# Performance work log

Hardware: AMD Instinct MI355X
Metric: run time of the kernel (lower is better)

The kernel has to match this reference:

```python
import jax, jax.numpy as jnp
import numpy as np

NUM_HEAD = 16
D = 1024
HEAD_DIM = D // NUM_HEAD
EPS = 1e-5


def setup_inputs() -> dict:
    key = jax.random.key(0)
    ks = jax.random.split(key, 7)
    B, S = 2, 2048
    s = 1.0 / np.sqrt(D)
    return {
        "x": jax.random.normal(ks[0], (B, S, D), dtype=jnp.float32),
        "wq": jax.random.uniform(ks[1], (D, D), jnp.float32, -s, s),
        "bq": jax.random.uniform(ks[2], (D,), jnp.float32, -s, s),
        "wk": jax.random.uniform(ks[3], (D, D), jnp.float32, -s, s),
        "bk": jax.random.uniform(ks[4], (D,), jnp.float32, -s, s),
        "wv": jax.random.uniform(ks[5], (D, D), jnp.float32, -s, s),
        "bv": jax.random.uniform(ks[6], (D,), jnp.float32, -s, s),
        "gamma": jnp.ones((D,), jnp.float32),
        "beta": jnp.zeros((D,), jnp.float32),
    }


def reference(x, wq, bq, wk, bk, wv, bv, gamma, beta):
    B, S, Dm = x.shape
    # Linear: x @ W^T + b (torch convention), then split heads -> [B, H, S, hd]
    def proj(w, b):
        y = jnp.einsum("bsd,ed->bse", x, w) + b
        return y.reshape(B, S, NUM_HEAD, HEAD_DIM).transpose(0, 2, 1, 3)

    q = proj(wq, bq)
    k = proj(wk, bk)
    v = proj(wv, bv)

    scores = jnp.einsum("bhqd,bhkd->bhqk", q, k) / np.sqrt(HEAD_DIM).astype(x.dtype)
    attn = jax.nn.softmax(scores, axis=-1)
    out = jnp.einsum("bhqk,bhkd->bhqd", attn, v)
    out = out.transpose(0, 2, 1, 3).reshape(B, S, Dm)

    out = out + x
    mu = jnp.mean(out, axis=-1, keepdims=True)
    var = jnp.var(out, axis=-1, keepdims=True)
    out = (out - mu) * jax.lax.rsqrt(var + EPS) * gamma + beta
    return out
```

## Files before the change

kernel.cpp:

```cpp
#include <hip/hip_runtime.h>

typedef unsigned short u16;
typedef unsigned int   u32;
typedef __bf16 bf16x8 __attribute__((ext_vector_type(8)));
typedef float  f32x4  __attribute__((ext_vector_type(4)));

#define D_MODEL 1024
#define SEQ     2048
#define NHEAD   16
#define HD      64
#define SOFTMAX_SCL 0.18033688011112042f

__device__ __forceinline__ u16 f2bf(float f) {
    u32 u;
    __builtin_memcpy(&u, &f, 4);
    u32 r = (u + 0x7fffu + ((u >> 16) & 1u)) >> 16;
    return (u16)r;
}
__device__ __forceinline__ float bf2f(u16 v) {
    u32 u = ((u32)v) << 16;
    float f;
    __builtin_memcpy(&f, &u, 4);
    return f;
}

__device__ __forceinline__ void async_copy16(const u16* g, u16* l) {
    __builtin_amdgcn_global_load_lds(
        (__attribute__((address_space(1))) void*)g,
        (__attribute__((address_space(3))) void*)l, 16, 0, 0);
}

__device__ __forceinline__ uint2 pack4(float a, float b, float c, float d) {
    uint2 r;
    r.x = (u32)f2bf(a) | ((u32)f2bf(b) << 16);
    r.y = (u32)f2bf(c) | ((u32)f2bf(d) << 16);
    return r;
}

#define NX4 ((2 * SEQ * D_MODEL) / 4)
#define NW4 ((D_MODEL * D_MODEL) / 4)
__global__ __launch_bounds__(256) void conv_all(
    const float* __restrict__ x,  const float* __restrict__ wq,
    const float* __restrict__ wk, const float* __restrict__ wv,
    u16* __restrict__ xb, u16* __restrict__ wqb,
    u16* __restrict__ wkb, u16* __restrict__ wvb)
{
    int i = blockIdx.x * 256 + threadIdx.x;
    const float* src; u16* dst; int off;
    if (i < NX4)            { src = x;  dst = xb;  off = i; }
    else if (i < NX4 + NW4) { src = wq; dst = wqb; off = i - NX4; }
    else if (i < NX4 + 2 * NW4) { src = wk; dst = wkb; off = i - NX4 - NW4; }
    else                    { src = wv; dst = wvb; off = i - NX4 - 2 * NW4; }
    float4 a = ((const float4*)src)[off];
    ushort4 o;
    o.x = f2bf(a.x); o.y = f2bf(a.y); o.z = f2bf(a.z); o.w = f2bf(a.w);
    ((ushort4*)dst)[off] = o;
}

__global__ __launch_bounds__(256) void qkv_gemm(
    const u16* __restrict__ xb,
    const u16* __restrict__ wqb, const float* __restrict__ bq,
    const u16* __restrict__ wkb, const float* __restrict__ bk,
    const u16* __restrict__ wvb, const float* __restrict__ bv,
    u16* __restrict__ qb, u16* __restrict__ kb, u16* __restrict__ vt)
{
    const int bid  = blockIdx.x;
    const int pair = bid % 24;
    const int by   = bid / 24;
    const int z    = pair >> 3;
    const int bx   = pair & 7;

    const u16* Ap; const u16* Bp;
    int m0, n0;
    if (z < 2) {
        Ap = (z == 1) ? wkb : wqb;  Bp = xb;
        m0 = bx * 128;
        n0 = by * 128;
    } else {
        Ap = xb;  Bp = wvb;
        m0 = by * 128;
        n0 = bx * 128;
    }

    __shared__ u16 As[128 * 64];
    __shared__ u16 Bs[128 * 64];

    const int tid  = threadIdx.x;
    const int wave = tid >> 6;
    const int lane = tid & 63;
    const int quad = lane >> 4;
    const int l16  = lane & 15;
    const int wm   = wave >> 1;
    const int wn   = wave & 1;
    const int swz  = l16 & 7;

    int rr[4], co[4];
#pragma unroll
    for (int t = 0; t < 4; ++t) {
        int ch = (wave * 4 + t) * 64 + lane;
        rr[t] = ch >> 3;
        co[t] = ((ch & 7) ^ (rr[t] & 7)) * 8;
    }

    f32x4 acc[4][4] = {};

    for (int kt = 0; kt < D_MODEL; kt += 64) {
        __syncthreads();
#pragma unroll
        for (int t = 0; t < 4; ++t) {
            int chbase = (wave * 4 + t) * 64;
            async_copy16(Ap + (size_t)(m0 + rr[t]) * D_MODEL + kt + co[t], As + chbase * 8);
            async_copy16(Bp + (size_t)(n0 + rr[t]) * D_MODEL + kt + co[t], Bs + chbase * 8);
        }
        __syncthreads();

#pragma unroll
        for (int kc = 0; kc < 2; ++kc) {
            bf16x8 af[4], bf_[4];
#pragma unroll
            for (int i = 0; i < 4; ++i)
                af[i] = *(const bf16x8*)&As[(wm * 64 + i * 16 + l16) * 64 + (((kc * 4 + quad) ^ swz) << 3)];
#pragma unroll
            for (int j = 0; j < 4; ++j)
                bf_[j] = *(const bf16x8*)&Bs[(wn * 64 + j * 16 + l16) * 64 + (((kc * 4 + quad) ^ swz) << 3)];
            __builtin_amdgcn_s_setprio(1);
#pragma unroll
            for (int i = 0; i < 4; ++i)
#pragma unroll
                for (int j = 0; j < 4; ++j)
                    acc[i][j] = __builtin_amdgcn_mfma_f32_16x16x32_bf16(af[i], bf_[j], acc[i][j], 0, 0, 0);
            __builtin_amdgcn_s_setprio(0);
        }
    }

    if (z < 2) {
        const int chunk_lo = (quad & 1) * 4;
        u16* out = (z == 1) ? kb : qb;
        const float* bi = (z == 1) ? bk : bq;
        const float scl = (z == 1) ? 1.0f : SOFTMAX_SCL;
        const int fblk = m0 + wm * 64;
#pragma unroll
        for (int i = 0; i < 4; ++i) {
            const int fb = fblk + i * 16 + quad * 4;
            float4 b4 = *(const float4*)&bi[fb];
            const int chunk = i * 2 + (quad >> 1);
#pragma unroll
            for (int j = 0; j < 4; ++j) {
                int token = n0 + wn * 64 + j * 16 + l16;
                uint2 pk = pack4((acc[i][j][0] + b4.x) * scl,
                                 (acc[i][j][1] + b4.y) * scl,
                                 (acc[i][j][2] + b4.z) * scl,
                                 (acc[i][j][3] + b4.w) * scl);
                size_t addr = (size_t)token * D_MODEL + fblk
                            + ((chunk ^ (token & 7)) << 3) + chunk_lo;
                *(uint2*)&out[addr] = pk;
            }
        }
    } else {
#pragma unroll
        for (int j = 0; j < 4; ++j) {
            int feat = n0 + wn * 64 + j * 16 + l16;
            float bias = bv[feat];
            int hh = feat >> 6, d = feat & 63;
            const size_t rowbase = ((size_t)hh * HD + d) * SEQ;
#pragma unroll
            for (int i = 0; i < 4; ++i) {
                int tok = m0 + wm * 64 + i * 16 + quad * 4;
                int b = tok >> 11, s = tok & 2047;
                const int nchunk = (i >> 1) * 4 + quad;
                const int nlo    = (i & 1) * 4;
                uint2 pk = pack4(acc[i][j][0] + bias, acc[i][j][1] + bias,
                                 acc[i][j][2] + bias, acc[i][j][3] + bias);
                size_t addr = (size_t)b * NHEAD * HD * SEQ + rowbase
                            + (s & ~63) + ((nchunk ^ (d & 7)) << 3) + nlo;
                *(uint2*)&vt[addr] = pk;
            }
        }
    }
}

__global__ __launch_bounds__(256) void attn_kernel(
    const u16* __restrict__ qb, const u16* __restrict__ kb, const u16* __restrict__ vtg,
    u16* __restrict__ abp, float* __restrict__ lsums)
{
    const int bid  = blockIdx.x;
    const int bh   = bid & 31;
    const int b    = bh >> 4;
    const int h    = bh & 15;
    const int q0   = ((bid >> 5) & 15) * 128;
    const int half = bid >> 9;

    const int tid  = threadIdx.x;
    const int wave = tid >> 6;
    const int lane = tid & 63;
    const int quad = lane >> 4;
    const int l16  = lane & 15;
    const int swz  = l16 & 7;

    __shared__ u16 Ks[2 * 4096];
    __shared__ u16 Vt[2 * 4096];

    const size_t kbase = (size_t)b * SEQ * D_MODEL + h * 64;
    const size_t vbase = (size_t)(b * NHEAD + h) * HD * SEQ;

    bf16x8 aq[2][2];
#pragma unroll
    for (int rb = 0; rb < 2; ++rb) {
        const int qrow = q0 + wave * 32 + rb * 16 + l16;
        const u16* qrp = qb + (size_t)qrow * D_MODEL + h * 64;
        aq[rb][0] = *(const bf16x8*)(qrp + ((quad ^ swz) << 3));
        aq[rb][1] = *(const bf16x8*)(qrp + (((4 + quad) ^ swz) << 3));
    }

    const int r0 = tid >> 3, r1 = (tid + 256) >> 3;
    const int cs8 = (tid & 7) * 8;
    const u16* kg0 = kb + kbase + (size_t)(half * 1024 + r0) * D_MODEL + cs8;
    const u16* kg1 = kb + kbase + (size_t)(half * 1024 + r1) * D_MODEL + cs8;
    const u16* vg0 = vtg + vbase + (size_t)r0 * SEQ + half * 1024 + cs8;
    const u16* vg1 = vtg + vbase + (size_t)r1 * SEQ + half * 1024 + cs8;
    const int wofs = wave * 512;

    f32x4 oacc[2][4] = {};
    float lsum[2] = {};

    async_copy16(kg0, Ks + wofs);
    async_copy16(kg1, Ks + 2048 + wofs);
    async_copy16(vg0, Vt + wofs);
    async_copy16(vg1, Vt + 2048 + wofs);
    kg0 += 64 * D_MODEL; kg1 += 64 * D_MODEL;
    vg0 += 64;           vg1 += 64;

    for (int t = 0; t < 16; ++t) {
        const int cur = (t & 1) << 12;
        const int nxt = cur ^ 4096;

        __builtin_amdgcn_s_barrier();
        if (t < 15) {
            async_copy16(kg0, Ks + nxt + wofs);
            async_copy16(kg1, Ks + nxt + 2048 + wofs);
            async_copy16(vg0, Vt + nxt + wofs);
            async_copy16(vg1, Vt + nxt + 2048 + wofs);
            kg0 += 64 * D_MODEL; kg1 += 64 * D_MODEL;
            vg0 += 64;           vg1 += 64;
            asm volatile("s_waitcnt vmcnt(4)" ::: "memory");
        } else {
            asm volatile("s_waitcnt vmcnt(0)" ::: "memory");
        }
        __builtin_amdgcn_s_barrier();

        const u16* Kc = Ks + cur;
        const u16* Vc = Vt + cur;

        f32x4 sacc[2][4] = {};
#pragma unroll
        for (int c = 0; c < 2; ++c) {
            bf16x8 bk_[4];
#pragma unroll
            for (int nb = 0; nb < 4; ++nb)
                bk_[nb] = *(const bf16x8*)&Kc[(nb * 16 + l16) * 64 + (((c * 4 + quad) ^ swz) << 3)];
            __builtin_amdgcn_s_setprio(1);
#pragma unroll
            for (int rb = 0; rb < 2; ++rb)
#pragma unroll
                for (int nb = 0; nb < 4; ++nb)
                    sacc[rb][nb] = __builtin_amdgcn_mfma_f32_16x16x32_bf16(bk_[nb], aq[rb][c], sacc[rb][nb], 0, 0, 0);
            __builtin_amdgcn_s_setprio(0);
        }

        bf16x8 ap[2][2];
#pragma unroll
        for (int rb = 0; rb < 2; ++rb) {
            u32 w[4][2];
#pragma unroll
            for (int nb = 0; nb < 4; ++nb) {
                float e0 = __builtin_amdgcn_exp2f(sacc[rb][nb][0]);
                float e1 = __builtin_amdgcn_exp2f(sacc[rb][nb][1]);
                float e2 = __builtin_amdgcn_exp2f(sacc[rb][nb][2]);
                float e3 = __builtin_amdgcn_exp2f(sacc[rb][nb][3]);
                lsum[rb] += (e0 + e1) + (e2 + e3);
                u32 b0, b1, b2, b3;
                __builtin_memcpy(&b0, &e0, 4); __builtin_memcpy(&b1, &e1, 4);
                __builtin_memcpy(&b2, &e2, 4); __builtin_memcpy(&b3, &e3, 4);
                w[nb][0] = __builtin_amdgcn_perm(b1, b0, 0x07060302);
                w[nb][1] = __builtin_amdgcn_perm(b3, b2, 0x07060302);
            }
            union { u32 d[4]; bf16x8 v; } u0, u1;
            u0.d[0] = w[0][0]; u0.d[1] = w[0][1]; u0.d[2] = w[1][0]; u0.d[3] = w[1][1];
            u1.d[0] = w[2][0]; u1.d[1] = w[2][1]; u1.d[2] = w[3][0]; u1.d[3] = w[3][1];
            ap[rb][0] = u0.v;
            ap[rb][1] = u1.v;
        }

#pragma unroll
        for (int c = 0; c < 2; ++c) {
            bf16x8 bv_[4];
#pragma unroll
            for (int nb = 0; nb < 4; ++nb)
                bv_[nb] = *(const bf16x8*)&Vc[(nb * 16 + l16) * 64 + (((c * 4 + quad) ^ swz) << 3)];
            __builtin_amdgcn_s_setprio(1);
#pragma unroll
            for (int rb = 0; rb < 2; ++rb)
#pragma unroll
                for (int nb = 0; nb < 4; ++nb)
                    oacc[rb][nb] = __builtin_amdgcn_mfma_f32_16x16x32_bf16(ap[rb][c], bv_[nb], oacc[rb][nb], 0, 0, 0);
            __builtin_amdgcn_s_setprio(0);
        }
    }

#pragma unroll
    for (int rb = 0; rb < 2; ++rb) {
        float s = lsum[rb];
        s += __shfl_xor(s, 16, 64);
        s += __shfl_xor(s, 32, 64);
        if (lane < 16)
            lsums[((size_t)bh * 2 + half) * SEQ + q0 + wave * 32 + rb * 16 + lane] = s;
#pragma unroll
        for (int r = 0; r < 4; ++r) {
            int row = q0 + wave * 32 + rb * 16 + quad * 4 + r;
#pragma unroll
            for (int nb = 0; nb < 4; ++nb) {
                int d = nb * 16 + l16;
                abp[(size_t)half * SEQ * 2 * D_MODEL
                    + ((size_t)b * SEQ + row) * D_MODEL + h * 64 + d] = f2bf(oacc[rb][nb][r]);
            }
        }
    }
}

__global__ __launch_bounds__(256) void add_ln(
    const u16* __restrict__ abp, const float* __restrict__ lsums,
    const float* __restrict__ x,
    const float* __restrict__ gamma, const float* __restrict__ beta,
    float* __restrict__ out)
{
    const int row = blockIdx.x;
    const int tid = threadIdx.x;
    const size_t rb = (size_t)row * D_MODEL;
    const int b = row >> 11, s = row & 2047;
    const int h = tid >> 4;
    const int bh = b * NHEAD + h;

    float l = lsums[(size_t)bh * 2 * SEQ + s] + lsums[((size_t)bh * 2 + 1) * SEQ + s];
    float inv = 1.0f / l;

    uint2 a0 = ((const uint2*)(abp + rb))[tid];
    uint2 a1 = ((const uint2*)(abp + (size_t)SEQ * 2 * D_MODEL + rb))[tid];
    float4 xb = ((const float4*)(x + rb))[tid];

    float v[4];
    v[0] = (bf2f((u16)(a0.x & 0xffff)) + bf2f((u16)(a1.x & 0xffff))) * inv + xb.x;
    v[1] = (bf2f((u16)(a0.x >> 16))    + bf2f((u16)(a1.x >> 16)))    * inv + xb.y;
    v[2] = (bf2f((u16)(a0.y & 0xffff)) + bf2f((u16)(a1.y & 0xffff))) * inv + xb.z;
    v[3] = (bf2f((u16)(a0.y >> 16))    + bf2f((u16)(a1.y >> 16)))    * inv + xb.w;

    float sm  = v[0] + v[1] + v[2] + v[3];
    float s2 = v[0]*v[0] + v[1]*v[1] + v[2]*v[2] + v[3]*v[3];
#pragma unroll
    for (int off = 1; off < 64; off <<= 1) {
        sm += __shfl_xor(sm, off, 64);
        s2 += __shfl_xor(s2, off, 64);
    }

    __shared__ float red[2][4];
    int wave = tid >> 6, lane = tid & 63;
    if (lane == 0) { red[0][wave] = sm; red[1][wave] = s2; }
    __syncthreads();
    float st  = red[0][0] + red[0][1] + red[0][2] + red[0][3];
    float s2t = red[1][0] + red[1][1] + red[1][2] + red[1][3];

    float mu   = st * (1.0f / D_MODEL);
    float var  = s2t * (1.0f / D_MODEL) - mu * mu;
    float rstd = rsqrtf(var + 1e-5f);

    float4 g  = ((const float4*)(gamma))[tid];
    float4 bt = ((const float4*)(beta))[tid];
    float4 o;
    o.x = (v[0] - mu) * rstd * g.x + bt.x;
    o.y = (v[1] - mu) * rstd * g.y + bt.y;
    o.z = (v[2] - mu) * rstd * g.z + bt.z;
    o.w = (v[3] - mu) * rstd * g.w + bt.w;
    ((float4*)(out + rb))[tid] = o;
}

extern "C" void kernel_launch(void* const* d_in, const int* in_sizes, int n_in,
                              void* d_out, int out_size, void* d_ws, size_t ws_size,
                              hipStream_t stream) {
    const float* x     = (const float*)d_in[0];
    const float* wq    = (const float*)d_in[1];
    const float* bq    = (const float*)d_in[2];
    const float* wk    = (const float*)d_in[3];
    const float* bk    = (const float*)d_in[4];
    const float* wv    = (const float*)d_in[5];
    const float* bv    = (const float*)d_in[6];
    const float* gamma = (const float*)d_in[7];
    const float* beta  = (const float*)d_in[8];
    float* outp = (float*)d_out;

    char* ws = (char*)d_ws;
    u16*   xb    = (u16*)(ws);
    u16*   wqb   = (u16*)(ws + ((size_t)8  << 20));
    u16*   wkb   = (u16*)(ws + ((size_t)10 << 20));
    u16*   wvb   = (u16*)(ws + ((size_t)12 << 20));
    u16*   qb    = (u16*)(ws + ((size_t)16 << 20));
    u16*   kb    = (u16*)(ws + ((size_t)24 << 20));
    u16*   vt    = (u16*)(ws + ((size_t)32 << 20));
    u16*   abp   = (u16*)(ws + ((size_t)40 << 20));
    float* lsums = (float*)(ws + ((size_t)56 << 20));

    conv_all<<<dim3((NX4 + 3 * NW4) / 256), 256, 0, stream>>>(
        x, wq, wk, wv, xb, wqb, wkb, wvb);
    qkv_gemm<<<dim3(24 * 32), 256, 0, stream>>>(xb, wqb, bq, wkb, bk, wvb, bv, qb, kb, vt);
    attn_kernel<<<dim3(1024), 256, 0, stream>>>(qb, kb, vt, abp, lsums);
    add_ln<<<dim3(2 * SEQ), 256, 0, stream>>>(abp, lsums, x, gamma, beta, outp);
}
```

Baseline: 183.0 us.

## Load K and V fragments directly from global memory, dropping LDS staging

Removes the double-buffered shared-memory staging of K and V tiles, with its async copies and barriers, in the attention kernel. Each wave now loads its K and V MFMA fragments straight from global memory into registers. This gets rid of LDS traffic and block-wide synchronisation. In exchange, all four waves redundantly fetch the same K/V tiles and lose the prefetch overlap, so the kernel depends on the L1/L2 caches and may stall on global load latency.

```diff
diff --git a/kernel.cpp b/kernel.cpp
--- a/kernel.cpp
+++ b/kernel.cpp
@@ -197,74 +197,54 @@
     const int l16  = lane & 15;
     const int swz  = l16 & 7;
 
-    __shared__ u16 Ks[2 * 4096];
-    __shared__ u16 Vt[2 * 4096];
-
     const size_t kbase = (size_t)b * SEQ * D_MODEL + h * 64;
     const size_t vbase = (size_t)(b * NHEAD + h) * HD * SEQ;
+
+    const int koff0 = ((quad) ^ swz) << 3;
+    const int koff1 = ((4 + quad) ^ swz) << 3;
 
     bf16x8 aq[2][2];
 #pragma unroll
     for (int rb = 0; rb < 2; ++rb) {
         const int qrow = q0 + wave * 32 + rb * 16 + l16;
         const u16* qrp = qb + (size_t)qrow * D_MODEL + h * 64;
-        aq[rb][0] = *(const bf16x8*)(qrp + ((quad ^ swz) << 3));
-        aq[rb][1] = *(const bf16x8*)(qrp + (((4 + quad) ^ swz) << 3));
-    }
-
-    const int r0 = tid >> 3, r1 = (tid + 256) >> 3;
-    const int cs8 = (tid & 7) * 8;
-    const u16* kg0 = kb + kbase + (size_t)(half * 1024 + r0) * D_MODEL + cs8;
-    const u16* kg1 = kb + kbase + (size_t)(half * 1024 + r1) * D_MODEL + cs8;
-    const u16* vg0 = vtg + vbase + (size_t)r0 * SEQ + half * 1024 + cs8;
-    const u16* vg1 = vtg + vbase + (size_t)r1 * SEQ + half * 1024 + cs8;
-    const int wofs = wave * 512;
+        aq[rb][0] = *(const bf16x8*)(qrp + koff0);
+        aq[rb][1] = *(const bf16x8*)(qrp + koff1);
+    }
+
+    const u16* kl = kb + kbase + (size_t)(half * 1024 + l16) * D_MODEL;
+    const u16* vl = vtg + vbase + (size_t)l16 * SEQ + half * 1024;
 
     f32x4 oacc[2][4] = {};
     float lsum[2] = {};
 
-    async_copy16(kg0, Ks + wofs);
-    async_copy16(kg1, Ks + 2048 + wofs);
-    async_copy16(vg0, Vt + wofs);
-    async_copy16(vg1, Vt + 2048 + wofs);
-    kg0 += 64 * D_MODEL; kg1 += 64 * D_MODEL;
-    vg0 += 64;           vg1 += 64;
-
     for (int t = 0; t < 16; ++t) {
-        const int cur = (t & 1) << 12;
-        const int nxt = cur ^ 4096;
-
-        __builtin_amdgcn_s_barrier();
-        if (t < 15) {
-            async_copy16(kg0, Ks + nxt + wofs);
-            async_copy16(kg1, Ks + nxt + 2048 + wofs);
-            async_copy16(vg0, Vt + nxt + wofs);
-            async_copy16(vg1, Vt + nxt + 2048 + wofs);
-            kg0 += 64 * D_MODEL; kg1 += 64 * D_MODEL;
-            vg0 += 64;           vg1 += 64;
-            asm volatile("s_waitcnt vmcnt(4)" ::: "memory");
-        } else {
-            asm volatile("s_waitcnt vmcnt(0)" ::: "memory");
-        }
-        __builtin_amdgcn_s_barrier();
-
-        const u16* Kc = Ks + cur;
-        const u16* Vc = Vt + cur;
+        bf16x8 kf[2][4];
+#pragma unroll
+        for (int nb = 0; nb < 4; ++nb) {
+            const u16* kr = kl + (size_t)(nb * 16) * D_MODEL;
+            kf[0][nb] = *(const bf16x8*)(kr + koff0);
+            kf[1][nb] = *(const bf16x8*)(kr + koff1);
+        }
 
         f32x4 sacc[2][4] = {};
 #pragma unroll
         for (int c = 0; c < 2; ++c) {
-            bf16x8 bk_[4];
-#pragma unroll
-            for (int nb = 0; nb < 4; ++nb)
-                bk_[nb] = *(const bf16x8*)&Kc[(nb * 16 + l16) * 64 + (((c * 4 + quad) ^ swz) << 3)];
             __builtin_amdgcn_s_setprio(1);
 #pragma unroll
             for (int rb = 0; rb < 2; ++rb)
 #pragma unroll
                 for (int nb = 0; nb < 4; ++nb)
-                    sacc[rb][nb] = __builtin_amdgcn_mfma_f32_16x16x32_bf16(bk_[nb], aq[rb][c], sacc[rb][nb], 0, 0, 0);
+                    sacc[rb][nb] = __builtin_amdgcn_mfma_f32_16x16x32_bf16(kf[c][nb], aq[rb][c], sacc[rb][nb], 0, 0, 0);
             __builtin_amdgcn_s_setprio(0);
+        }
+
+        bf16x8 vf[2][4];
+#pragma unroll
+        for (int nb = 0; nb < 4; ++nb) {
+            const u16* vr = vl + (size_t)(nb * 16) * SEQ;
+            vf[0][nb] = *(const bf16x8*)(vr + koff0);
+            vf[1][nb] = *(const bf16x8*)(vr + koff1);
         }
 
         bf16x8 ap[2][2];
@@ -293,18 +273,17 @@
 
 #pragma unroll
         for (int c = 0; c < 2; ++c) {
-            bf16x8 bv_[4];
-#pragma unroll
-            for (int nb = 0; nb < 4; ++nb)
-                bv_[nb] = *(const bf16x8*)&Vc[(nb * 16 + l16) * 64 + (((c * 4 + quad) ^ swz) << 3)];
             __builtin_amdgcn_s_setprio(1);
 #pragma unroll
             for (int rb = 0; rb < 2; ++rb)
 #pragma unroll
                 for (int nb = 0; nb < 4; ++nb)
-                    oacc[rb][nb] = __builtin_amdgcn_mfma_f32_16x16x32_bf16(ap[rb][c], bv_[nb], oacc[rb][nb], 0, 0, 0);
+                    oacc[rb][nb] = __builtin_amdgcn_mfma_f32_16x16x32_bf16(ap[rb][c], vf[c][nb], oacc[rb][nb], 0, 0, 0);
             __builtin_amdgcn_s_setprio(0);
         }
+
+        kl += 64 * D_MODEL;
+        vl += 64;
     }
 
 #pragma unroll
```

Measured after the change: 200.0 us. +9.3%, slower.
